# Kernel tuning notes

Hardware: AMD Instinct MI355X
Metric: run time of the kernel (lower is better)

The kernel has to match this reference:

```python
import jax, jax.numpy as jnp
import numpy as np

EMBED = 1024
ATTN = 1024

def setup_inputs() -> dict:
    key = jax.random.key(0)
    k1, k2, k3, k4 = jax.random.split(key, 4)
    x = jax.random.normal(k1, (32, 2048, EMBED), dtype=jnp.float32)
    W = jax.random.normal(k2, (EMBED, ATTN), dtype=jnp.float32) / np.sqrt(EMBED)
    b = jax.random.normal(k3, (ATTN,), dtype=jnp.float32) * 0.01
    ctx = jax.random.normal(k4, (ATTN,), dtype=jnp.float32)
    return {"x": x, "W": W, "b": b, "ctx": ctx}

def reference(x, W, b, ctx):
    # scores: [B, S] = tanh(x @ W + b) . ctx
    h = jnp.tanh(jnp.einsum('bse,ea->bsa', x, W) + b)
    scores = jnp.einsum('bsa,a->bs', h, ctx)
    weights = jax.nn.softmax(scores, axis=1)            # softmax over seq dim
    return jnp.einsum('bse,bs->be', x, weights)          # weighted sum pooling
```

## Files before the change

kernel.cpp:

```cpp
#include <hip/hip_runtime.h>
#include <hip/hip_bf16.h>

typedef _Float16 half8 __attribute__((ext_vector_type(8)));
typedef _Float16 half4 __attribute__((ext_vector_type(4)));
typedef float floatx4 __attribute__((ext_vector_type(4)));

#define EMBED 1024
#define SEQ   2048
#define BATCH 32
#define M_TOT (BATCH * SEQ)
#define KDIM  1024
#define NDIM  1024

#define GLOAD16(g, l) __builtin_amdgcn_global_load_lds(                      \
    (const __attribute__((address_space(1))) void*)(g),                      \
    (__attribute__((address_space(3))) void*)(l), 16, 0, 0)

__global__ void transpose_w_kernel(const float* __restrict__ W,
                                   _Float16* __restrict__ Wt) {
    __shared__ float t[32][33];
    const int kt = blockIdx.x * 32;
    const int nt = blockIdx.y * 32;
    #pragma unroll
    for (int i = 0; i < 4; ++i)
        t[threadIdx.y + 8 * i][threadIdx.x] =
            W[(size_t)(kt + threadIdx.y + 8 * i) * NDIM + nt + threadIdx.x];
    __syncthreads();
    #pragma unroll
    for (int i = 0; i < 4; ++i)
        Wt[(size_t)(nt + threadIdx.y + 8 * i) * KDIM + kt + threadIdx.x] =
            (_Float16)t[threadIdx.x][threadIdx.y + 8 * i];
}

__global__ void zero_kernel(float* __restrict__ scores, float* __restrict__ out) {
    const int i = blockIdx.x * 256 + threadIdx.x;
    if (i < M_TOT) scores[i] = 0.0f;
    if (i < BATCH * EMBED) out[i] = 0.0f;
}

__global__ __launch_bounds__(256) void cvt_x_kernel(const float* __restrict__ x,
                                                    _Float16* __restrict__ x16) {
    const size_t stride = (size_t)gridDim.x * 256 * 8;
    for (size_t i = ((size_t)blockIdx.x * 256 + threadIdx.x) * 8;
         i < (size_t)M_TOT * KDIM; i += stride) {
        const float4 a = *(const float4*)(x + i);
        const float4 b = *(const float4*)(x + i + 4);
        half8 h;
        h[0] = (_Float16)a.x; h[1] = (_Float16)a.y; h[2] = (_Float16)a.z; h[3] = (_Float16)a.w;
        h[4] = (_Float16)b.x; h[5] = (_Float16)b.y; h[6] = (_Float16)b.z; h[7] = (_Float16)b.w;
        *(half8*)(x16 + i) = h;
    }
}

__global__ __launch_bounds__(256, 3) void score_gemm3(
    const _Float16* __restrict__ x16, const _Float16* __restrict__ Wt,
    const float* __restrict__ bias, const float* __restrict__ ctx,
    float* __restrict__ scores) {
    __shared__ _Float16 As[2][128 * 32];
    __shared__ _Float16 Bs[2][128 * 32];

    const int nb = ((blockIdx.x & 7) << 9) | (blockIdx.x >> 3);
    const int bm = nb >> 3;
    const int bn = nb & 7;
    const int tid = threadIdx.x;
    const int lane = tid & 63;
    const int wid = tid >> 6;
    const int wm = wid >> 1;
    const int wn = wid & 1;

    const int jA0 = wid * 2;
    const int lrow = lane >> 2;
    const int gslot = (lane & 3) ^ (lrow & 3);
    const int gcol = gslot * 8;

    const _Float16* Ab = x16 + (size_t)(bm * 128) * KDIM;
    const _Float16* Bb = Wt  + (size_t)(bn * 128) * KDIM;

    floatx4 acc[4][4] = {};

    const int fslot = ((lane >> 4) ^ (lane & 3)) * 8;
    const int frow = lane & 15;

    #define STAGE(buf, kt)                                                        \
        {                                                                         \
            const int kc = (kt) * 32 + gcol;                                      \
            _Pragma("unroll")                                                     \
            for (int i = 0; i < 2; ++i) {                                         \
                const int j = jA0 + i;                                            \
                GLOAD16(Ab + (size_t)(j * 16 + lrow) * KDIM + kc, &As[buf][j * 512]); \
                GLOAD16(Bb + (size_t)(j * 16 + lrow) * KDIM + kc, &Bs[buf][j * 512]); \
            }                                                                     \
        }

    STAGE(0, 0);
    __syncthreads();

    for (int kt = 0; kt < KDIM / 32; ++kt) {
        const int cur = kt & 1;
        if (kt + 1 < KDIM / 32) STAGE(cur ^ 1, kt + 1);

        half8 afr[4], bfr[4];
        #pragma unroll
        for (int m = 0; m < 4; ++m)
            afr[m] = *(const half8*)&As[cur][(wm * 64 + m * 16 + frow) * 32 + fslot];
        #pragma unroll
        for (int n = 0; n < 4; ++n)
            bfr[n] = *(const half8*)&Bs[cur][(wn * 64 + n * 16 + frow) * 32 + fslot];

        #pragma unroll
        for (int m = 0; m < 4; ++m)
            #pragma unroll
            for (int n = 0; n < 4; ++n)
                acc[m][n] = __builtin_amdgcn_mfma_f32_16x16x32_f16(
                    afr[m], bfr[n], acc[m][n], 0, 0, 0);

        __syncthreads();
    }
    #undef STAGE

    float bv[4], cv[4];
    #pragma unroll
    for (int n = 0; n < 4; ++n) {
        const int col = bn * 128 + wn * 64 + n * 16 + (lane & 15);
        bv[n] = bias[col];
        cv[n] = ctx[col];
    }
    #pragma unroll
    for (int m = 0; m < 4; ++m) {
        #pragma unroll
        for (int j = 0; j < 4; ++j) {
            float partial = 0.0f;
            #pragma unroll
            for (int n = 0; n < 4; ++n) {
                const float v = acc[m][n][j] + bv[n];
                const float e = __expf(2.0f * v);
                const float t = 1.0f - 2.0f * __builtin_amdgcn_rcpf(e + 1.0f);
                partial += t * cv[n];
            }
            #pragma unroll
            for (int off = 1; off < 16; off <<= 1)
                partial += __shfl_xor(partial, off, 64);
            if ((lane & 15) == 0) {
                const int rowg = bm * 128 + wm * 64 + m * 16 + (lane >> 4) * 4 + j;
                atomicAdd(&scores[rowg], partial);
            }
        }
    }
}

__global__ __launch_bounds__(256) void score_gemm_f32(
    const float* __restrict__ A32p, const _Float16* __restrict__ Wt,
    const float* __restrict__ bias, const float* __restrict__ ctx,
    float* __restrict__ scores) {
    __shared__ _Float16 As[128 * 64];
    __shared__ _Float16 Bs[128 * 64];

    const int bid = blockIdx.x;
    const int bm = bid >> 3;
    const int bn = bid & 7;
    const int tid = threadIdx.x;
    const int lane = tid & 63;
    const int wid = tid >> 6;
    const int wm = wid >> 1;
    const int wn = wid & 1;

    const int c = tid & 7;
    const int r0 = tid >> 3;
    const int swz = (r0 & 7) << 3;
    const int wcol = (c * 8) ^ swz;

    float4 aF[4][2];
    int4   bR[4];

    #pragma unroll
    for (int i = 0; i < 4; ++i) {
        const int row = r0 + 32 * i;
        const float* p = A32p + (size_t)(bm * 128 + row) * KDIM + c * 8;
        aF[i][0] = *(const float4*)p;
        aF[i][1] = *(const float4*)(p + 4);
        bR[i] = *(const int4*)(Wt + (size_t)(bn * 128 + row) * KDIM + c * 8);
    }

    floatx4 acc[4][4] = {};

    for (int kt = 0; kt < KDIM / 64; ++kt) {
        __syncthreads();
        #pragma unroll
        for (int i = 0; i < 4; ++i) {
            const int row = r0 + 32 * i;
            half8 h;
            h[0] = (_Float16)aF[i][0].x; h[1] = (_Float16)aF[i][0].y;
            h[2] = (_Float16)aF[i][0].z; h[3] = (_Float16)aF[i][0].w;
            h[4] = (_Float16)aF[i][1].x; h[5] = (_Float16)aF[i][1].y;
            h[6] = (_Float16)aF[i][1].z; h[7] = (_Float16)aF[i][1].w;
            *(half8*)&As[row * 64 + wcol] = h;
            *(int4*)&Bs[row * 64 + wcol] = bR[i];
        }
        __syncthreads();

        if (kt + 1 < KDIM / 64) {
            #pragma unroll
            for (int i = 0; i < 4; ++i) {
                const int row = r0 + 32 * i;
                const float* p = A32p + (size_t)(bm * 128 + row) * KDIM + (kt + 1) * 64 + c * 8;
                aF[i][0] = *(const float4*)p;
                aF[i][1] = *(const float4*)(p + 4);
                bR[i] = *(const int4*)(Wt + (size_t)(bn * 128 + row) * KDIM + (kt + 1) * 64 + c * 8);
            }
        }

        #pragma unroll
        for (int s = 0; s < 2; ++s) {
            half8 afr[4], bfr[4];
            const int colr = s * 32 + (lane >> 4) * 8;
            #pragma unroll
            for (int m = 0; m < 4; ++m) {
                const int row = wm * 64 + m * 16 + (lane & 15);
                afr[m] = *(const half8*)&As[row * 64 + (colr ^ ((row & 7) << 3))];
            }
            #pragma unroll
            for (int n = 0; n < 4; ++n) {
                const int row = wn * 64 + n * 16 + (lane & 15);
                bfr[n] = *(const half8*)&Bs[row * 64 + (colr ^ ((row & 7) << 3))];
            }
            #pragma unroll
            for (int m = 0; m < 4; ++m)
                #pragma unroll
                for (int n = 0; n < 4; ++n)
                    acc[m][n] = __builtin_amdgcn_mfma_f32_16x16x32_f16(
                        afr[m], bfr[n], acc[m][n], 0, 0, 0);
        }
    }

    float bv[4], cv[4];
    #pragma unroll
    for (int n = 0; n < 4; ++n) {
        const int col = bn * 128 + wn * 64 + n * 16 + (lane & 15);
        bv[n] = bias[col];
        cv[n] = ctx[col];
    }
    #pragma unroll
    for (int m = 0; m < 4; ++m) {
        #pragma unroll
        for (int j = 0; j < 4; ++j) {
            float partial = 0.0f;
            #pragma unroll
            for (int n = 0; n < 4; ++n) {
                const float v = acc[m][n][j] + bv[n];
                const float e = __expf(2.0f * v);
                const float t = 1.0f - 2.0f * __builtin_amdgcn_rcpf(e + 1.0f);
                partial += t * cv[n];
            }
            #pragma unroll
            for (int off = 1; off < 16; off <<= 1)
                partial += __shfl_xor(partial, off, 64);
            if ((lane & 15) == 0) {
                const int rowg = bm * 128 + wm * 64 + m * 16 + (lane >> 4) * 4 + j;
                atomicAdd(&scores[rowg], partial);
            }
        }
    }
}

__global__ void softmax_kernel(const float* __restrict__ scores,
                               float* __restrict__ weights) {
    const int bb = blockIdx.x;
    const int tid = threadIdx.x;
    const float* s = scores + (size_t)bb * SEQ;
    float* w = weights + (size_t)bb * SEQ;

    __shared__ float red[8];

    float v[8];
    float mx = -1e30f;
    #pragma unroll
    for (int i = 0; i < 8; ++i) {
        v[i] = s[tid + i * 256];
        mx = fmaxf(mx, v[i]);
    }
    #pragma unroll
    for (int off = 1; off < 64; off <<= 1)
        mx = fmaxf(mx, __shfl_xor(mx, off, 64));
    const int wv = tid >> 6;
    if ((tid & 63) == 0) red[wv] = mx;
    __syncthreads();
    mx = fmaxf(fmaxf(red[0], red[1]), fmaxf(red[2], red[3]));

    float sum = 0.0f;
    #pragma unroll
    for (int i = 0; i < 8; ++i) {
        v[i] = __expf(v[i] - mx);
        sum += v[i];
    }
    #pragma unroll
    for (int off = 1; off < 64; off <<= 1)
        sum += __shfl_xor(sum, off, 64);
    if ((tid & 63) == 0) red[4 + wv] = sum;
    __syncthreads();
    sum = red[4] + red[5] + red[6] + red[7];
    const float inv = 1.0f / sum;
    #pragma unroll
    for (int i = 0; i < 8; ++i)
        w[tid + i * 256] = v[i] * inv;
}

__global__ __launch_bounds__(256) void pool_kernel(const float* __restrict__ x,
                                                   const float* __restrict__ weights,
                                                   float* __restrict__ out) {
    const int bb = blockIdx.x >> 4;
    const int sc = blockIdx.x & 15;
    const int tid = threadIdx.x;

    const float4* xb = (const float4*)(x + (size_t)bb * SEQ * EMBED) +
                       (size_t)(sc * 128) * (EMBED / 4) + tid;
    const float* wb = weights + (size_t)bb * SEQ + sc * 128;

    float ax = 0.f, ay = 0.f, az = 0.f, aw = 0.f;
    #pragma unroll 4
    for (int s = 0; s < 128; ++s) {
        const float wgt = wb[s];
        const float4 xv = xb[(size_t)s * (EMBED / 4)];
        ax += wgt * xv.x; ay += wgt * xv.y; az += wgt * xv.z; aw += wgt * xv.w;
    }
    float* o = out + (size_t)bb * EMBED + tid * 4;
    atomicAdd(o + 0, ax);
    atomicAdd(o + 1, ay);
    atomicAdd(o + 2, az);
    atomicAdd(o + 3, aw);
}

__global__ __launch_bounds__(256) void pool16_kernel(const _Float16* __restrict__ x16,
                                                     const float* __restrict__ weights,
                                                     float* __restrict__ out) {
    const int bb = blockIdx.x >> 4;
    const int sc = blockIdx.x & 15;
    const int tid = threadIdx.x;

    const _Float16* xb = x16 + (size_t)bb * SEQ * EMBED +
                         (size_t)(sc * 128) * EMBED + tid * 4;
    const float* wb = weights + (size_t)bb * SEQ + sc * 128;

    float ax = 0.f, ay = 0.f, az = 0.f, aw = 0.f;
    #pragma unroll 4
    for (int s = 0; s < 128; ++s) {
        const float wgt = wb[s];
        const half4 h = *(const half4*)(xb + (size_t)s * EMBED);
        ax += wgt * (float)h[0]; ay += wgt * (float)h[1];
        az += wgt * (float)h[2]; aw += wgt * (float)h[3];
    }
    float* o = out + (size_t)bb * EMBED + tid * 4;
    atomicAdd(o + 0, ax);
    atomicAdd(o + 1, ay);
    atomicAdd(o + 2, az);
    atomicAdd(o + 3, aw);
}

extern "C" void kernel_launch(void* const* d_in, const int* in_sizes, int n_in,
                              void* d_out, int out_size, void* d_ws, size_t ws_size,
                              hipStream_t stream) {
    const float* x   = (const float*)d_in[0];
    const float* W   = (const float*)d_in[1];
    const float* b   = (const float*)d_in[2];
    const float* ctx = (const float*)d_in[3];
    float* out = (float*)d_out;

    char* ws = (char*)d_ws;
    _Float16* Wt      = (_Float16*)ws;
    float*    scores  = (float*)(ws + (2u << 20));
    float*    weights = (float*)(ws + (2u << 20) + (256u << 10));
    _Float16* x16     = (_Float16*)(ws + (4u << 20));

    const size_t need = (4ull << 20) + ((size_t)M_TOT * KDIM * 2);
    const bool fast = ws_size >= need;

    hipLaunchKernelGGL(transpose_w_kernel, dim3(32, 32), dim3(32, 8), 0, stream, W, Wt);
    hipLaunchKernelGGL(zero_kernel, dim3(M_TOT / 256), dim3(256), 0, stream, scores, out);

    if (fast) {
        hipLaunchKernelGGL(cvt_x_kernel, dim3(4096), dim3(256), 0, stream, x, x16);
        hipLaunchKernelGGL(score_gemm3, dim3(4096), dim3(256), 0, stream,
                           x16, Wt, b, ctx, scores);
    } else {
        hipLaunchKernelGGL(score_gemm_f32, dim3(4096), dim3(256), 0, stream,
                           x, Wt, b, ctx, scores);
    }

    hipLaunchKernelGGL(softmax_kernel, dim3(BATCH), dim3(256), 0, stream, scores, weights);

    if (fast) {
        hipLaunchKernelGGL(pool16_kernel, dim3(BATCH * 16), dim3(256), 0, stream,
                           x16, weights, out);
    } else {
        hipLaunchKernelGGL(pool_kernel, dim3(BATCH * 16), dim3(256), 0, stream,
                           x, weights, out);
    }
}
```

Before: 292.7 us.

## Enlarge score GEMM tile to 256x256x64 with 8 waves and setprio

Replaces the 128x128x32 score GEMM with a 256x256 block tile using 512 threads (8 waves, each 128x64) and K-steps of 64, with a new XOR-swizzled LDS layout. The bigger tile raises arithmetic intensity per byte loaded from global memory and halves the number of K-loop barriers. It also raises MFMA issue priority around the compute section. In exchange each wave holds 32 accumulators (more registers) and LDS use rises to 128KB per block, which limits occupancy.

```diff
diff --git a/kernel.cpp b/kernel.cpp
--- a/kernel.cpp
+++ b/kernel.cpp
@@ -52,96 +52,101 @@
     }
 }
 
-__global__ __launch_bounds__(256, 3) void score_gemm3(
+__global__ __launch_bounds__(512, 2) void score_gemm4(
     const _Float16* __restrict__ x16, const _Float16* __restrict__ Wt,
     const float* __restrict__ bias, const float* __restrict__ ctx,
     float* __restrict__ scores) {
-    __shared__ _Float16 As[2][128 * 32];
-    __shared__ _Float16 Bs[2][128 * 32];
-
-    const int nb = ((blockIdx.x & 7) << 9) | (blockIdx.x >> 3);
-    const int bm = nb >> 3;
-    const int bn = nb & 7;
+    __shared__ _Float16 As[2][256 * 64];
+    __shared__ _Float16 Bs[2][256 * 64];
+
     const int tid = threadIdx.x;
     const int lane = tid & 63;
-    const int wid = tid >> 6;
-    const int wm = wid >> 1;
-    const int wn = wid & 1;
-
-    const int jA0 = wid * 2;
-    const int lrow = lane >> 2;
-    const int gslot = (lane & 3) ^ (lrow & 3);
-    const int gcol = gslot * 8;
-
-    const _Float16* Ab = x16 + (size_t)(bm * 128) * KDIM;
-    const _Float16* Bb = Wt  + (size_t)(bn * 128) * KDIM;
-
-    floatx4 acc[4][4] = {};
-
-    const int fslot = ((lane >> 4) ^ (lane & 3)) * 8;
+    const int w = tid >> 6;
+    const int wm = w >> 2;
+    const int wn = w & 3;
+
+    const int nb = ((blockIdx.x & 7) << 7) | (blockIdx.x >> 3);
+    const int bm = nb >> 2;
+    const int bn = nb & 3;
+
+    const int srow  = lane >> 3;
+    const int sslot = (lane & 7) ^ srow;
+    const _Float16* Ab = x16 + (size_t)(bm * 256) * KDIM;
+    const _Float16* Bb = Wt  + (size_t)(bn * 256) * KDIM;
+
+    #define STAGE(buf, kt)                                                         \
+        {                                                                          \
+            _Pragma("unroll")                                                      \
+            for (int i = 0; i < 4; ++i) {                                          \
+                const int j = i * 8 + w;                                           \
+                const size_t go = (size_t)(j * 8 + srow) * KDIM + (kt) * 64 + sslot * 8; \
+                GLOAD16(Ab + go, &As[buf][j * 512]);                               \
+                GLOAD16(Bb + go, &Bs[buf][j * 512]);                               \
+            }                                                                      \
+        }
+
     const int frow = lane & 15;
-
-    #define STAGE(buf, kt)                                                        \
-        {                                                                         \
-            const int kc = (kt) * 32 + gcol;                                      \
-            _Pragma("unroll")                                                     \
-            for (int i = 0; i < 2; ++i) {                                         \
-                const int j = jA0 + i;                                            \
-                GLOAD16(Ab + (size_t)(j * 16 + lrow) * KDIM + kc, &As[buf][j * 512]); \
-                GLOAD16(Bb + (size_t)(j * 16 + lrow) * KDIM + kc, &Bs[buf][j * 512]); \
-            }                                                                     \
-        }
+    const int fsw  = frow & 7;
+    const int fhi  = lane >> 4;
+
+    floatx4 acc[8][4] = {};
 
     STAGE(0, 0);
     __syncthreads();
 
-    for (int kt = 0; kt < KDIM / 32; ++kt) {
+    for (int kt = 0; kt < 16; ++kt) {
         const int cur = kt & 1;
-        if (kt + 1 < KDIM / 32) STAGE(cur ^ 1, kt + 1);
-
-        half8 afr[4], bfr[4];
+        if (kt < 15) STAGE(cur ^ 1, kt + 1);
+
         #pragma unroll
-        for (int m = 0; m < 4; ++m)
-            afr[m] = *(const half8*)&As[cur][(wm * 64 + m * 16 + frow) * 32 + fslot];
-        #pragma unroll
-        for (int n = 0; n < 4; ++n)
-            bfr[n] = *(const half8*)&Bs[cur][(wn * 64 + n * 16 + frow) * 32 + fslot];
-
-        #pragma unroll
-        for (int m = 0; m < 4; ++m)
-            #pragma unroll
-            for (int n = 0; n < 4; ++n)
-                acc[m][n] = __builtin_amdgcn_mfma_f32_16x16x32_f16(
-                    afr[m], bfr[n], acc[m][n], 0, 0, 0);
-
+        for (int ks = 0; ks < 2; ++ks) {
+            const int sp = ks * 4 + fhi;
+            half8 bfr[4];
+            #pragma unroll
+            for (int ni = 0; ni < 4; ++ni) {
+                const int r = wn * 64 + ni * 16 + frow;
+                bfr[ni] = *(const half8*)&Bs[cur][r * 64 + ((sp ^ fsw) * 8)];
+            }
+            __builtin_amdgcn_s_setprio(1);
+            #pragma unroll
+            for (int mi = 0; mi < 8; ++mi) {
+                const int r = wm * 128 + mi * 16 + frow;
+                const half8 a = *(const half8*)&As[cur][r * 64 + ((sp ^ fsw) * 8)];
+                #pragma unroll
+                for (int ni = 0; ni < 4; ++ni)
+                    acc[mi][ni] = __builtin_amdgcn_mfma_f32_16x16x32_f16(
+                        a, bfr[ni], acc[mi][ni], 0, 0, 0);
+            }
+            __builtin_amdgcn_s_setprio(0);
+        }
         __syncthreads();
     }
     #undef STAGE
 
     float bv[4], cv[4];
     #pragma unroll
-    for (int n = 0; n < 4; ++n) {
-        const int col = bn * 128 + wn * 64 + n * 16 + (lane & 15);
-        bv[n] = bias[col];
-        cv[n] = ctx[col];
-    }
-    #pragma unroll
-    for (int m = 0; m < 4; ++m) {
+    for (int ni = 0; ni < 4; ++ni) {
+        const int col = bn * 256 + wn * 64 + ni * 16 + frow;
+        bv[ni] = bias[col];
+        cv[ni] = ctx[col];
+    }
+    #pragma unroll
+    for (int mi = 0; mi < 8; ++mi) {
         #pragma unroll
         for (int j = 0; j < 4; ++j) {
             float partial = 0.0f;
             #pragma unroll
-            for (int n = 0; n < 4; ++n) {
-                const float v = acc[m][n][j] + bv[n];
+            for (int ni = 0; ni < 4; ++ni) {
+                const float v = acc[mi][ni][j] + bv[ni];
                 const float e = __expf(2.0f * v);
                 const float t = 1.0f - 2.0f * __builtin_amdgcn_rcpf(e + 1.0f);
-                partial += t * cv[n];
+                partial += t * cv[ni];
             }
             #pragma unroll
             for (int off = 1; off < 16; off <<= 1)
                 partial += __shfl_xor(partial, off, 64);
-            if ((lane & 15) == 0) {
-                const int rowg = bm * 128 + wm * 64 + m * 16 + (lane >> 4) * 4 + j;
+            if (frow == 0) {
+                const int rowg = bm * 256 + wm * 128 + mi * 16 + fhi * 4 + j;
                 atomicAdd(&scores[rowg], partial);
             }
         }
@@ -378,7 +383,7 @@
 
     if (fast) {
         hipLaunchKernelGGL(cvt_x_kernel, dim3(4096), dim3(256), 0, stream, x, x16);
-        hipLaunchKernelGGL(score_gemm3, dim3(4096), dim3(256), 0, stream,
+        hipLaunchKernelGGL(score_gemm4, dim3(1024), dim3(512), 0, stream,
                            x16, Wt, b, ctx, scores);
     } else {
         hipLaunchKernelGGL(score_gemm_f32, dim3(4096), dim3(256), 0, stream,
```

Result: no change. 293.1 us (+0.2%).

## Triple-buffer GEMM LDS staging with explicit vmcnt waits and MFMA priority

Applied to the files above, without the earlier changes.

The score GEMM moves from double to triple-buffered LDS staging via global_load_lds. Loads now run two k-tiles ahead, and explicit s_waitcnt vmcnt counts replace the blanket __syncthreads waits. The MFMA block is wrapped in s_setprio to favour matrix issue. LDS use rises to 48KB per block, which may limit occupancy at 3 blocks per CU, and the hand-coded vmcnt values depend on the exact number of loads issued per stage.

```diff
diff --git a/kernel.cpp b/kernel.cpp
--- a/kernel.cpp
+++ b/kernel.cpp
@@ -52,12 +52,12 @@
     }
 }
 
-__global__ __launch_bounds__(256, 3) void score_gemm3(
+__global__ __launch_bounds__(256, 3) void score_gemm7(
     const _Float16* __restrict__ x16, const _Float16* __restrict__ Wt,
     const float* __restrict__ bias, const float* __restrict__ ctx,
     float* __restrict__ scores) {
-    __shared__ _Float16 As[2][128 * 32];
-    __shared__ _Float16 Bs[2][128 * 32];
+    __shared__ _Float16 As[3][128 * 32];
+    __shared__ _Float16 Bs[3][128 * 32];
 
     const int nb = ((blockIdx.x & 7) << 9) | (blockIdx.x >> 3);
     const int bm = nb >> 3;
@@ -92,30 +92,49 @@
             }                                                                     \
         }
 
+    #define COMPUTE(buf)                                                          \
+        {                                                                         \
+            half8 afr[4], bfr[4];                                                 \
+            _Pragma("unroll")                                                     \
+            for (int m = 0; m < 4; ++m)                                           \
+                afr[m] = *(const half8*)&As[buf][(wm * 64 + m * 16 + frow) * 32 + fslot]; \
+            _Pragma("unroll")                                                     \
+            for (int n = 0; n < 4; ++n)                                           \
+                bfr[n] = *(const half8*)&Bs[buf][(wn * 64 + n * 16 + frow) * 32 + fslot]; \
+            __builtin_amdgcn_s_setprio(1);                                        \
+            _Pragma("unroll")                                                     \
+            for (int m = 0; m < 4; ++m)                                           \
+                _Pragma("unroll")                                                 \
+                for (int n = 0; n < 4; ++n)                                       \
+                    acc[m][n] = __builtin_amdgcn_mfma_f32_16x16x32_f16(           \
+                        afr[m], bfr[n], acc[m][n], 0, 0, 0);                      \
+            __builtin_amdgcn_s_setprio(0);                                        \
+        }
+
     STAGE(0, 0);
-    __syncthreads();
-
-    for (int kt = 0; kt < KDIM / 32; ++kt) {
-        const int cur = kt & 1;
-        if (kt + 1 < KDIM / 32) STAGE(cur ^ 1, kt + 1);
-
-        half8 afr[4], bfr[4];
-        #pragma unroll
-        for (int m = 0; m < 4; ++m)
-            afr[m] = *(const half8*)&As[cur][(wm * 64 + m * 16 + frow) * 32 + fslot];
-        #pragma unroll
-        for (int n = 0; n < 4; ++n)
-            bfr[n] = *(const half8*)&Bs[cur][(wn * 64 + n * 16 + frow) * 32 + fslot];
-
-        #pragma unroll
-        for (int m = 0; m < 4; ++m)
-            #pragma unroll
-            for (int n = 0; n < 4; ++n)
-                acc[m][n] = __builtin_amdgcn_mfma_f32_16x16x32_f16(
-                    afr[m], bfr[n], acc[m][n], 0, 0, 0);
-
-        __syncthreads();
-    }
+    STAGE(1, 1);
+
+    int cur = 0;
+    int stg = 2;
+    for (int kt = 0; kt < KDIM / 32 - 2; ++kt) {
+        STAGE(stg, kt + 2);
+        asm volatile("s_waitcnt vmcnt(8)" ::: "memory");
+        __builtin_amdgcn_s_barrier();
+        COMPUTE(cur);
+        __builtin_amdgcn_s_barrier();
+        cur = (cur == 2) ? 0 : cur + 1;
+        stg = (stg == 2) ? 0 : stg + 1;
+    }
+    asm volatile("s_waitcnt vmcnt(4)" ::: "memory");
+    __builtin_amdgcn_s_barrier();
+    COMPUTE(cur);
+    __builtin_amdgcn_s_barrier();
+    cur = (cur == 2) ? 0 : cur + 1;
+    asm volatile("s_waitcnt vmcnt(0)" ::: "memory");
+    __builtin_amdgcn_s_barrier();
+    COMPUTE(cur);
+
+    #undef COMPUTE
     #undef STAGE
 
     float bv[4], cv[4];
@@ -378,7 +397,7 @@
 
     if (fast) {
         hipLaunchKernelGGL(cvt_x_kernel, dim3(4096), dim3(256), 0, stream, x, x16);
-        hipLaunchKernelGGL(score_gemm3, dim3(4096), dim3(256), 0, stream,
+        hipLaunchKernelGGL(score_gemm7, dim3(4096), dim3(256), 0, stream,
                            x16, Wt, b, ctx, scores);
     } else {
         hipLaunchKernelGGL(score_gemm_f32, dim3(4096), dim3(256), 0, stream,
```

New measurement: 306.6 us. +4.8%, slower.
